# Kernel tuning notes

Hardware: AMD Instinct MI355X
Metric: run time of the kernel (lower is better)

The kernel has to match this reference:

```python
import jax, jax.numpy as jnp
import numpy as np

B, T, C, NH = 8, 512, 512, 8
HD = C // NH

def _layernorm(x, g, b, eps=1e-5):
    mu = jnp.mean(x, axis=-1, keepdims=True)
    var = jnp.var(x, axis=-1, keepdims=True)
    return (x - mu) * jax.lax.rsqrt(var + eps) * g + b

def setup_inputs() -> dict:
    key = jax.random.key(0)
    ks = jax.random.split(key, 5)
    return {
        "x": jax.random.normal(ks[0], (B, T, C), jnp.float32),
        "w_attn": jax.random.normal(ks[1], (3 * C, C), jnp.float32) * (1.0 / np.sqrt(C)),
        "b_attn": jnp.zeros((3 * C,), jnp.float32),
        "w_proj": jax.random.normal(ks[2], (C, C), jnp.float32) * (1.0 / np.sqrt(C)),
        "b_proj": jnp.zeros((C,), jnp.float32),
        "q_gamma": jnp.ones((C,), jnp.float32),
        "q_beta": jnp.zeros((C,), jnp.float32),
        "k_gamma": jnp.ones((C,), jnp.float32),
        "k_beta": jnp.zeros((C,), jnp.float32),
        "rel_emb": jax.random.normal(ks[3], (T, C), jnp.float32) * 0.02,
    }

def reference(x, w_attn, b_attn, w_proj, b_proj, q_gamma, q_beta, k_gamma, k_beta, rel_emb):
    b, t, c = x.shape
    # QKV projection (torch Linear: x @ W.T + b)
    qkv = x @ w_attn.T + b_attn                       # [B,T,3C]
    q, k, v = jnp.split(qkv, 3, axis=-1)
    # per-stream LayerNorm over full embedding dim (q_ln/k_ln = LayerNorm(n_embd))
    q = _layernorm(q, q_gamma, q_beta)
    k = _layernorm(k, k_gamma, k_beta)
    # split heads -> [B,NH,T,HD]
    q = q.reshape(b, t, NH, HD).transpose(0, 2, 1, 3)
    k = k.reshape(b, t, NH, HD).transpose(0, 2, 1, 3)
    v = v.reshape(b, t, NH, HD).transpose(0, 2, 1, 3)
    # relative-position bias: gather rel_emb[|i-j|] -> [T,T,NH,HD]
    idx = jnp.abs(jnp.arange(t)[None, :] - jnp.arange(t)[:, None])  # [T,T] int
    rel = rel_emb[idx].reshape(t, t, NH, HD)
    rel_bias = jnp.einsum("bhqd,qkhd->bhqk", q, rel)  # [B,NH,T,T]
    scale = 1.0 / np.sqrt(HD)
    scores = (jnp.einsum("bhqd,bhkd->bhqk", q, k) + rel_bias) * scale
    causal = jnp.tril(jnp.ones((t, t), bool))
    scores = jnp.where(causal[None, None], scores, jnp.finfo(scores.dtype).min)
    att = jax.nn.softmax(scores, axis=-1)
    y = jnp.einsum("bhqk,bhkd->bhqd", att, v)         # [B,NH,T,HD]
    y = y.transpose(0, 2, 1, 3).reshape(b, t, c)
    return y @ w_proj.T + b_proj
```

## Files before the change

kernel.cpp:

```cpp
#include <hip/hip_runtime.h>
#include <hip/hip_bf16.h>
#include <cstddef>

#define BB 8
#define TT 512
#define CC 512
#define NHH 8
#define HDD 64

typedef __attribute__((ext_vector_type(8))) short short8;
typedef __attribute__((ext_vector_type(4))) float f32x4;

__device__ __forceinline__ unsigned short f2bf(float f) {
    unsigned u = __float_as_uint(f);
    u += 0x7FFFu + ((u >> 16) & 1u);
    return (unsigned short)(u >> 16);
}
__device__ __forceinline__ float bf2f(unsigned short h) {
    return __uint_as_float(((unsigned)h) << 16);
}

__global__ __launch_bounds__(256) void cvt_all_k(
    const float* __restrict__ x, const float* __restrict__ wa,
    const float* __restrict__ wp, const float* __restrict__ rel,
    unsigned short* __restrict__ Xb, unsigned short* __restrict__ Wqb,
    unsigned short* __restrict__ Wpb, unsigned short* __restrict__ Relb)
{
    const int bidx = blockIdx.x;
    const float* in;
    unsigned short* out;
    int base;
    if (bidx < 2048)      { in = x;   out = Xb;   base = bidx; }
    else if (bidx < 2816) { in = wa;  out = Wqb;  base = bidx - 2048; }
    else if (bidx < 3072) { in = wp;  out = Wpb;  base = bidx - 2816; }
    else                  { in = rel; out = Relb; base = bidx - 3072; }
    const int i = base * 1024 + threadIdx.x * 4;
    const float4 v = *(const float4*)(in + i);
    unsigned short tmp[4] = {f2bf(v.x), f2bf(v.y), f2bf(v.z), f2bf(v.w)};
    *(uint2*)(out + i) = *(const uint2*)tmp;
}

__global__ __launch_bounds__(256, 2) void gemm_qkv_mfma(
    const unsigned short* __restrict__ Xb, const unsigned short* __restrict__ Wb,
    const float* __restrict__ bias, unsigned short* __restrict__ qkbuf,
    unsigned short* __restrict__ VT)
{
    __shared__ __align__(16) unsigned short lds[128 * 136];

    const int tid = threadIdx.x;
    const int w = tid >> 6, lane = tid & 63;
    const int c = lane & 15, quad = lane >> 4;
    const int wm = w >> 1, wn = w & 1;
    const int bm = blockIdx.y * 128, bn = blockIdx.x * 128;

    const unsigned short* pp[8];
#pragma unroll
    for (int l = 0; l < 8; ++l) {
        const int ci = w * 8 + l;
        if (ci < 16) {
            const int m16 = ci >> 1, kk = ci & 1;
            pp[l] = Xb + (size_t)(bm + m16 * 16 + c) * 512 + kk * 32 + quad * 8;
        } else {
            const int cb = ci - 16, n16 = cb >> 1, kk = cb & 1;
            pp[l] = Wb + (size_t)(bn + n16 * 16 + c) * 512 + kk * 32 + quad * 8;
        }
    }

    f32x4 acc[4][4];
#pragma unroll
    for (int i = 0; i < 4; ++i)
#pragma unroll
        for (int j = 0; j < 4; ++j) acc[i][j] = (f32x4){0.f, 0.f, 0.f, 0.f};

    short8 pre[8];
#pragma unroll
    for (int l = 0; l < 8; ++l) pre[l] = *(const short8*)pp[l];

    for (int k0 = 0; k0 < 512; k0 += 64) {
        __syncthreads();
#pragma unroll
        for (int l = 0; l < 8; ++l)
            *(short8*)&lds[(w * 8 + l) * 512 + lane * 8] = pre[l];
        __syncthreads();
        if (k0 + 64 < 512) {
#pragma unroll
            for (int l = 0; l < 8; ++l)
                pre[l] = *(const short8*)(pp[l] + k0 + 64);
        }
#pragma unroll
        for (int kk = 0; kk < 2; ++kk) {
            short8 af[4], bfr[4];
#pragma unroll
            for (int i = 0; i < 4; ++i)
                af[i] = *(const short8*)&lds[((wm * 4 + i) * 2 + kk) * 512 + lane * 8];
#pragma unroll
            for (int j = 0; j < 4; ++j)
                bfr[j] = *(const short8*)&lds[(16 + (wn * 4 + j) * 2 + kk) * 512 + lane * 8];
#pragma unroll
            for (int i = 0; i < 4; ++i)
#pragma unroll
                for (int j = 0; j < 4; ++j)
                    acc[i][j] = __builtin_amdgcn_mfma_f32_16x16x32_bf16(
                        af[i], bfr[j], acc[i][j], 0, 0, 0);
        }
    }

    float bj[4];
#pragma unroll
    for (int j = 0; j < 4; ++j) bj[j] = bias[bn + wn * 64 + j * 16 + c];

    if (bn < 1024) {
#pragma unroll
        for (int i = 0; i < 4; ++i)
#pragma unroll
            for (int j = 0; j < 4; ++j) {
                const int n = bn + wn * 64 + j * 16 + c;
#pragma unroll
                for (int r = 0; r < 4; ++r) {
                    const int m = bm + wm * 64 + i * 16 + quad * 4 + r;
                    qkbuf[(size_t)m * 1024 + n] = f2bf(acc[i][j][r] + bj[j]);
                }
            }
    } else {
        __syncthreads();
#pragma unroll
        for (int i = 0; i < 4; ++i)
#pragma unroll
            for (int j = 0; j < 4; ++j) {
                const int col = wn * 64 + j * 16 + c;
                const int row0 = wm * 64 + i * 16 + quad * 4;
                unsigned short t4[4];
#pragma unroll
                for (int r = 0; r < 4; ++r) t4[r] = f2bf(acc[i][j][r] + bj[j]);
                *(uint2*)&lds[col * 136 + row0] = *(const uint2*)t4;
            }
        __syncthreads();
        const int bi = bm >> 9, tb = bm & 511;
        const int hd0 = bn - 1024;
#pragma unroll
        for (int l = 0; l < 8; ++l) {
            const int idx = l * 256 + tid;
            const int col = idx >> 4, grp = idx & 15;
            const short8 v = *(const short8*)&lds[col * 136 + grp * 8];
            const int hd = hd0 + col, h = hd >> 6, d = hd & 63;
            *(short8*)(VT + ((size_t)(bi * NHH + h) * HDD + d) * TT + tb + grp * 8) = v;
        }
    }
}

__global__ __launch_bounds__(256) void ln_k(
    const unsigned short* __restrict__ qkbuf,
    const float* __restrict__ qg, const float* __restrict__ qb,
    const float* __restrict__ kg, const float* __restrict__ kb,
    unsigned short* __restrict__ Qh, unsigned short* __restrict__ Kh)
{
    const int wv = threadIdx.x >> 6, lane = threadIdx.x & 63;
    const int row = blockIdx.x * 4 + wv;
    const int bi = row >> 9, t = row & 511;
    const unsigned short* base = qkbuf + (size_t)row * 1024;

#pragma unroll
    for (int s = 0; s < 2; ++s) {
        const short8 v8 = *(const short8*)(base + s * 512 + lane * 8);
        float vf[8];
#pragma unroll
        for (int i = 0; i < 8; ++i) vf[i] = bf2f(((const unsigned short*)&v8)[i]);
        float sum = 0.f, sq = 0.f;
#pragma unroll
        for (int i = 0; i < 8; ++i) { sum += vf[i]; sq += vf[i] * vf[i]; }
#pragma unroll
        for (int off = 1; off < 64; off <<= 1) {
            sum += __shfl_xor(sum, off);
            sq += __shfl_xor(sq, off);
        }
        const float mu = sum * (1.f / 512.f);
        const float var = sq * (1.f / 512.f) - mu * mu;
        const float rsg = rsqrtf(var + 1e-5f);
        const float* gam = (s ? kg : qg) + lane * 8;
        const float* bet = (s ? kb : qb) + lane * 8;
        const float4 g0 = *(const float4*)gam, g1 = *(const float4*)(gam + 4);
        const float4 b0 = *(const float4*)bet, b1 = *(const float4*)(bet + 4);
        const float gv[8] = {g0.x, g0.y, g0.z, g0.w, g1.x, g1.y, g1.z, g1.w};
        const float bv[8] = {b0.x, b0.y, b0.z, b0.w, b1.x, b1.y, b1.z, b1.w};
        const float osc = s ? 1.0f : 0.125f;
        unsigned short o8[8];
#pragma unroll
        for (int i = 0; i < 8; ++i)
            o8[i] = f2bf(((vf[i] - mu) * rsg * gv[i] + bv[i]) * osc);
        unsigned short* outp = s ? Kh : Qh;
        *(short8*)(outp + ((size_t)(bi * NHH + (lane >> 3)) * TT + t) * HDD
                   + (lane & 7) * 8) = *(const short8*)o8;
    }
}

#define RD_BODY(nr_)                                                            \
    {                                                                           \
        const short8 br0 = *(const short8*)&Rels[((nr_) * 2 + 0) * 512 + lane * 8]; \
        const short8 br1 = *(const short8*)&Rels[((nr_) * 2 + 1) * 512 + lane * 8]; \
        f32x4 a2 = (f32x4){0.f, 0.f, 0.f, 0.f};                                 \
        a2 = __builtin_amdgcn_mfma_f32_16x16x32_bf16(aq0, br0, a2, 0, 0, 0);    \
        a2 = __builtin_amdgcn_mfma_f32_16x16x32_bf16(aq1, br1, a2, 0, 0, 0);    \
        const int colw = (mbase + (nr_) * 16 + c) & 127;                        \
        _Pragma("unroll")                                                       \
        for (int r = 0; r < 4; ++r)                                             \
            RDs[w][(quad * 4 + r) * 132 + colw] = f2bf(a2[r]);                  \
    }

__global__ __launch_bounds__(256, 2) void attn_k(
    const unsigned short* __restrict__ Qh, const unsigned short* __restrict__ Kh,
    const unsigned short* __restrict__ VT, const unsigned short* __restrict__ Relb,
    unsigned short* __restrict__ Yb)
{
    __shared__ __align__(16) unsigned short Ks[8 * 512];
    __shared__ __align__(16) unsigned short Vs[8 * 512];
    __shared__ __align__(16) unsigned short Rels[16 * 512];
    __shared__ __align__(16) unsigned short Ps[4][16 * 72];
    __shared__ __align__(16) unsigned short RDs[4][16 * 132];

    const int tid = threadIdx.x;
    const int w = tid >> 6;
    const int lane = tid & 63;
    const int c = lane & 15;
    const int quad = lane >> 4;

    const int bid = blockIdx.x;
    const int bit0 = bid & 1, bit8 = (bid >> 8) & 1;
    const int s_ = bit0 ^ bit8;
    const int q0 = (bid >> 1) & 7;
    const int qt = s_ ? 7 - q0 : q0;
    const int h = (bid >> 4) & 7;
    const int b = ((bid >> 7) & 1) | (bit8 << 1) | (bit0 << 2);
    const int i0 = qt * 64;

    const unsigned short* Qbase = Qh + (size_t)(b * NHH + h) * TT * HDD;
    const unsigned short* Kbase = Kh + (size_t)(b * NHH + h) * TT * HDD;
    const unsigned short* Vbase = VT + (size_t)(b * NHH + h) * HDD * TT;
    const unsigned short* Rbase = Relb + h * HDD;

    const unsigned short* qp = Qbase + (size_t)(i0 + w * 16 + c) * HDD + quad * 8;
    const short8 aq0 = *(const short8*)qp;
    const short8 aq1 = *(const short8*)(qp + 32);

#pragma unroll
    for (int kk = 0; kk < 2; ++kk) {
        const unsigned short* gp = Kbase + (size_t)(w * 16 + c) * HDD + kk * 32 + quad * 8;
        *(short8*)&Ks[(w * 2 + kk) * 512 + lane * 8] = *(const short8*)gp;
    }
#pragma unroll
    for (int js = 0; js < 2; ++js) {
        const unsigned short* gp = Vbase + (size_t)(w * 16 + c) * TT + js * 32 + quad * 8;
        *(short8*)&Vs[(w * 2 + js) * 512 + lane * 8] = *(const short8*)gp;
    }
    {
        const int mb0 = i0 - 63;
#pragma unroll
        for (int sb = 0; sb < 2; ++sb) {
#pragma unroll
            for (int kk = 0; kk < 2; ++kk) {
                const int n16 = w * 2 + sb;
                int mrow = mb0 + n16 * 16 + c;
                mrow = mrow < 0 ? 0 : (mrow > 511 ? 511 : mrow);
                *(short8*)&Rels[(n16 * 2 + kk) * 512 + lane * 8] =
                    *(const short8*)(Rbase + (size_t)mrow * CC + kk * 32 + quad * 8);
            }
        }
    }

    f32x4 oacc[4];
    float m_i[4], l_i[4];
#pragma unroll
    for (int r = 0; r < 4; ++r) { m_i[r] = -1e30f; l_i[r] = 0.f; }
#pragma unroll
    for (int nd = 0; nd < 4; ++nd) oacc[nd] = (f32x4){0.f, 0.f, 0.f, 0.f};

    __syncthreads();

    for (int jt = 0; jt <= qt; ++jt) {
        const int j0 = jt * 64;

        short8 pK0, pK1, pV0, pV1, pR0, pR1;
        if (jt < qt) {
            const int j1 = j0 + 64;
            const unsigned short* kp = Kbase + (size_t)(j1 + w * 16 + c) * HDD + quad * 8;
            pK0 = *(const short8*)kp;
            pK1 = *(const short8*)(kp + 32);
            const unsigned short* vp = Vbase + (size_t)(w * 16 + c) * TT + j1 + quad * 8;
            pV0 = *(const short8*)vp;
            pV1 = *(const short8*)(vp + 32);
            int mr = i0 - j1 - 63 + w * 16 + c;
            mr = mr < 0 ? 0 : (mr > 511 ? 511 : mr);
            const unsigned short* rp = Rbase + (size_t)mr * CC + quad * 8;
            pR0 = *(const short8*)rp;
            pR1 = *(const short8*)(rp + 32);
        }

        f32x4 sAcc[4];
#pragma unroll
        for (int ns = 0; ns < 4; ++ns) {
            const short8 bk0 = *(const short8*)&Ks[(ns * 2 + 0) * 512 + lane * 8];
            const short8 bk1 = *(const short8*)&Ks[(ns * 2 + 1) * 512 + lane * 8];
            f32x4 a2 = (f32x4){0.f, 0.f, 0.f, 0.f};
            a2 = __builtin_amdgcn_mfma_f32_16x16x32_bf16(aq0, bk0, a2, 0, 0, 0);
            a2 = __builtin_amdgcn_mfma_f32_16x16x32_bf16(aq1, bk1, a2, 0, 0, 0);
            sAcc[ns] = a2;
        }
        const int mbase = i0 - j0 - 63;
        if (jt == 0) {
#pragma unroll
            for (int nr = 0; nr < 8; ++nr) RD_BODY(nr)
        } else {
#pragma unroll
            for (int nr = 0; nr < 4; ++nr) RD_BODY(nr)
        }

        const int dbase = i0 - j0;
        float sc[4][4];
#pragma unroll
        for (int ns = 0; ns < 4; ++ns) {
#pragma unroll
            for (int r = 0; r < 4; ++r) {
                const int r16 = quad * 4 + r;
                const int jc = ns * 16 + c;
                const int dp = (dbase + w * 16 + r16 - jc) & 127;
                const float rdv = bf2f(RDs[w][r16 * 132 + dp]);
                sc[ns][r] = sAcc[ns][r] + rdv;
            }
        }
        if (jt == qt) {
#pragma unroll
            for (int ns = 0; ns < 4; ++ns)
#pragma unroll
                for (int r = 0; r < 4; ++r)
                    if (ns * 16 + c > w * 16 + quad * 4 + r) sc[ns][r] = -1e30f;
        }

        float alpha[4];
#pragma unroll
        for (int r = 0; r < 4; ++r) {
            float m = fmaxf(fmaxf(sc[0][r], sc[1][r]), fmaxf(sc[2][r], sc[3][r]));
#pragma unroll
            for (int off = 1; off < 16; off <<= 1) m = fmaxf(m, __shfl_xor(m, off));
            const float mn = fmaxf(m_i[r], m);
            alpha[r] = __expf(m_i[r] - mn);
            m_i[r] = mn;
        }
        float rs[4] = {0.f, 0.f, 0.f, 0.f};
#pragma unroll
        for (int ns = 0; ns < 4; ++ns) {
#pragma unroll
            for (int r = 0; r < 4; ++r) {
                const float p = __expf(sc[ns][r] - m_i[r]);
                rs[r] += p;
                Ps[w][(quad * 4 + r) * 72 + ns * 16 + c] = f2bf(p);
            }
        }
#pragma unroll
        for (int r = 0; r < 4; ++r) {
#pragma unroll
            for (int off = 1; off < 16; off <<= 1) rs[r] += __shfl_xor(rs[r], off);
            l_i[r] = l_i[r] * alpha[r] + rs[r];
        }
#pragma unroll
        for (int nd = 0; nd < 4; ++nd)
#pragma unroll
            for (int r = 0; r < 4; ++r) oacc[nd][r] *= alpha[r];

        const short8 ap0 = *(const short8*)&Ps[w][c * 72 + 0 * 32 + quad * 8];
        const short8 ap1 = *(const short8*)&Ps[w][c * 72 + 1 * 32 + quad * 8];
#pragma unroll
        for (int nd = 0; nd < 4; ++nd) {
            const short8 bv0 = *(const short8*)&Vs[(nd * 2 + 0) * 512 + lane * 8];
            const short8 bv1 = *(const short8*)&Vs[(nd * 2 + 1) * 512 + lane * 8];
            oacc[nd] = __builtin_amdgcn_mfma_f32_16x16x32_bf16(ap0, bv0, oacc[nd], 0, 0, 0);
            oacc[nd] = __builtin_amdgcn_mfma_f32_16x16x32_bf16(ap1, bv1, oacc[nd], 0, 0, 0);
        }

        if (jt < qt) {
            __syncthreads();
#pragma unroll
            for (int kk = 0; kk < 2; ++kk)
                *(short8*)&Ks[(w * 2 + kk) * 512 + lane * 8] = (kk ? pK1 : pK0);
#pragma unroll
            for (int js = 0; js < 2; ++js)
                *(short8*)&Vs[(w * 2 + js) * 512 + lane * 8] = (js ? pV1 : pV0);
#pragma unroll
            for (int kk = 0; kk < 2; ++kk)
                *(short8*)&Rels[(w * 2 + kk) * 512 + lane * 8] = (kk ? pR1 : pR0);
            __syncthreads();
        }
    }

#pragma unroll
    for (int r = 0; r < 4; ++r) {
        const float inv = 1.f / l_i[r];
        const int trow = i0 + w * 16 + quad * 4 + r;
        unsigned short* yb = Yb + ((size_t)b * TT + trow) * CC + h * HDD;
#pragma unroll
        for (int nd = 0; nd < 4; ++nd)
            yb[nd * 16 + c] = f2bf(oacc[nd][r] * inv);
    }
}

__global__ __launch_bounds__(256, 2) void gemm_proj_mfma(
    const unsigned short* __restrict__ Yb, const unsigned short* __restrict__ Wp,
    const float* __restrict__ bias, float* __restrict__ out)
{
    __shared__ __align__(16) unsigned short lds[24 * 512];

    const int tid = threadIdx.x;
    const int w = tid >> 6, lane = tid & 63;
    const int c = lane & 15, quad = lane >> 4;
    const int wm = w >> 1, wn = w & 1;
    const int bm = blockIdx.y * 64, bn = blockIdx.x * 128;

    const unsigned short* pp[6];
#pragma unroll
    for (int l = 0; l < 6; ++l) {
        const int ci = w * 6 + l;
        if (ci < 8) {
            const int m16 = ci >> 1, kk = ci & 1;
            pp[l] = Yb + (size_t)(bm + m16 * 16 + c) * 512 + kk * 32 + quad * 8;
        } else {
            const int cb = ci - 8, n16 = cb >> 1, kk = cb & 1;
            pp[l] = Wp + (size_t)(bn + n16 * 16 + c) * 512 + kk * 32 + quad * 8;
        }
    }

    f32x4 acc[2][4];
#pragma unroll
    for (int i = 0; i < 2; ++i)
#pragma unroll
        for (int j = 0; j < 4; ++j) acc[i][j] = (f32x4){0.f, 0.f, 0.f, 0.f};

    short8 pre[6];
#pragma unroll
    for (int l = 0; l < 6; ++l) pre[l] = *(const short8*)pp[l];

    for (int k0 = 0; k0 < 512; k0 += 64) {
        __syncthreads();
#pragma unroll
        for (int l = 0; l < 6; ++l)
            *(short8*)&lds[(w * 6 + l) * 512 + lane * 8] = pre[l];
        __syncthreads();
        if (k0 + 64 < 512) {
#pragma unroll
            for (int l = 0; l < 6; ++l)
                pre[l] = *(const short8*)(pp[l] + k0 + 64);
        }
#pragma unroll
        for (int kk = 0; kk < 2; ++kk) {
            short8 af[2], bfr[4];
#pragma unroll
            for (int i = 0; i < 2; ++i)
                af[i] = *(const short8*)&lds[((wm * 2 + i) * 2 + kk) * 512 + lane * 8];
#pragma unroll
            for (int j = 0; j < 4; ++j)
                bfr[j] = *(const short8*)&lds[(8 + (wn * 4 + j) * 2 + kk) * 512 + lane * 8];
#pragma unroll
            for (int i = 0; i < 2; ++i)
#pragma unroll
                for (int j = 0; j < 4; ++j)
                    acc[i][j] = __builtin_amdgcn_mfma_f32_16x16x32_bf16(
                        af[i], bfr[j], acc[i][j], 0, 0, 0);
        }
    }

#pragma unroll
    for (int j = 0; j < 4; ++j) {
        const int n = bn + wn * 64 + j * 16 + c;
        const float bj = bias[n];
#pragma unroll
        for (int i = 0; i < 2; ++i)
#pragma unroll
            for (int r = 0; r < 4; ++r) {
                const int m = bm + wm * 32 + i * 16 + quad * 4 + r;
                out[(size_t)m * 512 + n] = acc[i][j][r] + bj;
            }
    }
}

extern "C" void kernel_launch(void* const* d_in, const int* in_sizes, int n_in,
                              void* d_out, int out_size, void* d_ws, size_t ws_size,
                              hipStream_t stream)
{
    const float* x      = (const float*)d_in[0];
    const float* w_attn = (const float*)d_in[1];
    const float* b_attn = (const float*)d_in[2];
    const float* w_proj = (const float*)d_in[3];
    const float* b_proj = (const float*)d_in[4];
    const float* q_g    = (const float*)d_in[5];
    const float* q_b    = (const float*)d_in[6];
    const float* k_g    = (const float*)d_in[7];
    const float* k_b    = (const float*)d_in[8];
    const float* rel    = (const float*)d_in[9];
    float* out = (float*)d_out;

    unsigned short* qkbuf = (unsigned short*)d_ws;
    unsigned short* Qh   = qkbuf + (size_t)4096 * 1024;
    unsigned short* Kh   = Qh + (size_t)4096 * 512;
    unsigned short* VT   = Kh + (size_t)4096 * 512;
    unsigned short* Relb = VT + (size_t)4096 * 512;
    unsigned short* Xb   = Relb + (size_t)512 * 512;
    unsigned short* Wqb  = Xb + (size_t)4096 * 512;
    unsigned short* Wpb  = Wqb + (size_t)1536 * 512;
    unsigned short* Yb   = qkbuf;

    cvt_all_k<<<3328, 256, 0, stream>>>(x, w_attn, w_proj, rel, Xb, Wqb, Wpb, Relb);
    gemm_qkv_mfma<<<dim3(12, 32), 256, 0, stream>>>(Xb, Wqb, b_attn, qkbuf, VT);
    ln_k<<<1024, 256, 0, stream>>>(qkbuf, q_g, q_b, k_g, k_b, Qh, Kh);
    attn_k<<<512, 256, 0, stream>>>(Qh, Kh, VT, Relb, Yb);
    gemm_proj_mfma<<<dim3(4, 64), 256, 0, stream>>>(Yb, Wpb, b_proj, out);
}
```

Before: 139.5 us.

## Fuse QKV GEMM with LayerNorm and fp32 X conversion, restructure projection GEMM

Drops the separate X bf16 conversion and the LayerNorm kernel. The new QKV kernel reads fp32 x, converts it in-register while staging into LDS, and loads B fragments straight from global memory into registers with double buffering. Each block computes a full 512-wide stream slab so it can apply LayerNorm (including the softmax scale folded with log2e) before writing Q/K/VT. The attention softmax switches to exp2f to match that folded scale, and the projection GEMM is restructured the same way. The cost is fewer, heavier blocks (192 blocks at 1 per CU) with high register pressure, which risks lower occupancy.

New measurement: 144.3 us. +3.4%, slower.

```diff
diff --git a/kernel.cpp b/kernel.cpp
--- a/kernel.cpp
+++ b/kernel.cpp
@@ -20,176 +20,238 @@
     return __uint_as_float(((unsigned)h) << 16);
 }
 
-__global__ __launch_bounds__(256) void cvt_all_k(
-    const float* __restrict__ x, const float* __restrict__ wa,
-    const float* __restrict__ wp, const float* __restrict__ rel,
-    unsigned short* __restrict__ Xb, unsigned short* __restrict__ Wqb,
-    unsigned short* __restrict__ Wpb, unsigned short* __restrict__ Relb)
+__global__ __launch_bounds__(256) void cvt_w_k(
+    const float* __restrict__ wa, const float* __restrict__ wp,
+    const float* __restrict__ rel,
+    unsigned short* __restrict__ Wqb, unsigned short* __restrict__ Wpb,
+    unsigned short* __restrict__ Relb)
 {
     const int bidx = blockIdx.x;
     const float* in;
     unsigned short* out;
     int base;
-    if (bidx < 2048)      { in = x;   out = Xb;   base = bidx; }
-    else if (bidx < 2816) { in = wa;  out = Wqb;  base = bidx - 2048; }
-    else if (bidx < 3072) { in = wp;  out = Wpb;  base = bidx - 2816; }
-    else                  { in = rel; out = Relb; base = bidx - 3072; }
+    if (bidx < 768)       { in = wa;  out = Wqb;  base = bidx; }
+    else if (bidx < 1024) { in = wp;  out = Wpb;  base = bidx - 768; }
+    else                  { in = rel; out = Relb; base = bidx - 1024; }
     const int i = base * 1024 + threadIdx.x * 4;
     const float4 v = *(const float4*)(in + i);
     unsigned short tmp[4] = {f2bf(v.x), f2bf(v.y), f2bf(v.z), f2bf(v.w)};
     *(uint2*)(out + i) = *(const uint2*)tmp;
 }
 
-__global__ __launch_bounds__(256, 2) void gemm_qkv_mfma(
-    const unsigned short* __restrict__ Xb, const unsigned short* __restrict__ Wb,
-    const float* __restrict__ bias, unsigned short* __restrict__ qkbuf,
+#define QSTAGE_A()                                                            \
+    __syncthreads();                                                          \
+    _Pragma("unroll")                                                         \
+    for (int l = 0; l < 2; ++l) {                                             \
+        unsigned short t8[8];                                                 \
+        _Pragma("unroll")                                                     \
+        for (int e = 0; e < 4; ++e) {                                         \
+            t8[e] = f2bf(ap[l][0][e]);                                        \
+            t8[4 + e] = f2bf(ap[l][1][e]);                                    \
+        }                                                                     \
+        *(short8*)&smem[dstA[l]] = *(const short8*)t8;                        \
+    }                                                                         \
+    __syncthreads();
+
+#define QLOADA(koff)                                                          \
+    _Pragma("unroll")                                                         \
+    for (int l = 0; l < 2; ++l) {                                             \
+        ap[l][0] = *(const f32x4*)(srcA[l] + (koff));                         \
+        ap[l][1] = *(const f32x4*)(srcA[l] + (koff) + 4);                     \
+    }
+
+#define QLOADB(bN, koff)                                                      \
+    _Pragma("unroll")                                                         \
+    for (int kk = 0; kk < 2; ++kk)                                            \
+        _Pragma("unroll")                                                     \
+        for (int j = 0; j < 8; ++j)                                           \
+            bN[kk * 8 + j] =                                                  \
+                *(const short8*)(Bb + (size_t)j * 8192 + kk * 32 + (koff));
+
+#define QCOMPUTE(bN)                                                          \
+    _Pragma("unroll")                                                         \
+    for (int kk = 0; kk < 2; ++kk) {                                          \
+        short8 af[4];                                                         \
+        _Pragma("unroll")                                                     \
+        for (int i = 0; i < 4; ++i)                                           \
+            af[i] = *(const short8*)&smem[((i << 1) | kk) * 512 + lane * 8];  \
+        _Pragma("unroll")                                                     \
+        for (int j = 0; j < 8; ++j)                                           \
+            _Pragma("unroll")                                                 \
+            for (int i = 0; i < 4; ++i)                                       \
+                acc[i][j] = __builtin_amdgcn_mfma_f32_16x16x32_bf16(          \
+                    af[i], bN[kk * 8 + j], acc[i][j], 0, 0, 0);               \
+    }
+
+__global__ __launch_bounds__(256, 1) void qkvln_k(
+    const float* __restrict__ x, const unsigned short* __restrict__ Wqb,
+    const float* __restrict__ b_attn,
+    const float* __restrict__ qg, const float* __restrict__ qb,
+    const float* __restrict__ kg, const float* __restrict__ kb,
+    unsigned short* __restrict__ Qh, unsigned short* __restrict__ Kh,
     unsigned short* __restrict__ VT)
 {
-    __shared__ __align__(16) unsigned short lds[128 * 136];
+    __shared__ __align__(16) unsigned short smem[512 * 68];
 
     const int tid = threadIdx.x;
     const int w = tid >> 6, lane = tid & 63;
     const int c = lane & 15, quad = lane >> 4;
-    const int wm = w >> 1, wn = w & 1;
-    const int bm = blockIdx.y * 128, bn = blockIdx.x * 128;
-
-    const unsigned short* pp[8];
-#pragma unroll
-    for (int l = 0; l < 8; ++l) {
-        const int ci = w * 8 + l;
-        if (ci < 16) {
-            const int m16 = ci >> 1, kk = ci & 1;
-            pp[l] = Xb + (size_t)(bm + m16 * 16 + c) * 512 + kk * 32 + quad * 8;
-        } else {
-            const int cb = ci - 16, n16 = cb >> 1, kk = cb & 1;
-            pp[l] = Wb + (size_t)(bn + n16 * 16 + c) * 512 + kk * 32 + quad * 8;
-        }
-    }
-
-    f32x4 acc[4][4];
+
+    const int strm = blockIdx.x >> 6;
+    const int slab = blockIdx.x & 63;
+    const int row0 = slab * 64;
+    const int bi = row0 >> 9, trow0 = row0 & 511;
+
+    const float* srcA[2];
+    int dstA[2];
+#pragma unroll
+    for (int l = 0; l < 2; ++l) {
+        const int idx = l * 256 + tid;
+        const int fr = idx >> 6, li = idx & 63;
+        srcA[l] = x + (size_t)(row0 + (fr >> 1) * 16 + (li & 15)) * 512
+                    + (fr & 1) * 32 + (li >> 4) * 8;
+        dstA[l] = fr * 512 + li * 8;
+    }
+    const unsigned short* Bb =
+        Wqb + (size_t)(strm * 512 + w * 128 + c) * 512 + quad * 8;
+
+    f32x4 acc[4][8];
 #pragma unroll
     for (int i = 0; i < 4; ++i)
 #pragma unroll
-        for (int j = 0; j < 4; ++j) acc[i][j] = (f32x4){0.f, 0.f, 0.f, 0.f};
-
-    short8 pre[8];
-#pragma unroll
-    for (int l = 0; l < 8; ++l) pre[l] = *(const short8*)pp[l];
-
-    for (int k0 = 0; k0 < 512; k0 += 64) {
+        for (int j = 0; j < 8; ++j) acc[i][j] = (f32x4){0.f, 0.f, 0.f, 0.f};
+
+    f32x4 ap[2][2];
+    short8 b0[16], b1[16];
+    QLOADA(0);
+    QLOADB(b0, 0);
+
+#pragma unroll
+    for (int kp = 0; kp < 4; ++kp) {
+        const int ka = kp * 128;
+        QSTAGE_A();
+        QLOADA(ka + 64);
+        QLOADB(b1, ka + 64);
+        QCOMPUTE(b0);
+        QSTAGE_A();
+        if (kp < 3) {
+            QLOADA(ka + 128);
+            QLOADB(b0, ka + 128);
+        }
+        QCOMPUTE(b1);
+    }
+
+    {
+        const int gcb = strm * 512 + w * 128;
+#pragma unroll
+        for (int j = 0; j < 8; ++j) {
+            const float bj = b_attn[gcb + j * 16 + c];
+#pragma unroll
+            for (int i = 0; i < 4; ++i)
+#pragma unroll
+                for (int r = 0; r < 4; ++r) acc[i][j][r] += bj;
+        }
+    }
+
+    if (strm < 2) {
+        float s1[4][4], s2[4][4];
+#pragma unroll
+        for (int i = 0; i < 4; ++i)
+#pragma unroll
+            for (int r = 0; r < 4; ++r) {
+                float a1 = 0.f, a2 = 0.f;
+#pragma unroll
+                for (int j = 0; j < 8; ++j) {
+                    const float v = acc[i][j][r];
+                    a1 += v;
+                    a2 += v * v;
+                }
+#pragma unroll
+                for (int off = 1; off < 16; off <<= 1) {
+                    a1 += __shfl_xor(a1, off);
+                    a2 += __shfl_xor(a2, off);
+                }
+                s1[i][r] = a1;
+                s2[i][r] = a2;
+            }
         __syncthreads();
-#pragma unroll
-        for (int l = 0; l < 8; ++l)
-            *(short8*)&lds[(w * 8 + l) * 512 + lane * 8] = pre[l];
+        if (c == 0) {
+#pragma unroll
+            for (int i = 0; i < 4; ++i)
+#pragma unroll
+                for (int r = 0; r < 4; ++r)
+                    ((float2*)smem)[w * 64 + i * 16 + quad * 4 + r] =
+                        make_float2(s1[i][r], s2[i][r]);
+        }
         __syncthreads();
-        if (k0 + 64 < 512) {
-#pragma unroll
-            for (int l = 0; l < 8; ++l)
-                pre[l] = *(const short8*)(pp[l] + k0 + 64);
-        }
-#pragma unroll
-        for (int kk = 0; kk < 2; ++kk) {
-            short8 af[4], bfr[4];
+        float rsg[4][4], nmu[4][4];
+#pragma unroll
+        for (int i = 0; i < 4; ++i)
+#pragma unroll
+            for (int r = 0; r < 4; ++r) {
+                float a1 = 0.f, a2 = 0.f;
+#pragma unroll
+                for (int ww = 0; ww < 4; ++ww) {
+                    const float2 t =
+                        ((const float2*)smem)[ww * 64 + i * 16 + quad * 4 + r];
+                    a1 += t.x;
+                    a2 += t.y;
+                }
+                const float mu = a1 * (1.f / 512.f);
+                const float var = a2 * (1.f / 512.f) - mu * mu;
+                const float rs = rsqrtf(var + 1e-5f);
+                rsg[i][r] = rs;
+                nmu[i][r] = -mu * rs;
+            }
+        const float osc = (strm == 0) ? 0.1803368801f : 1.0f;
+        const float* gam = (strm == 0) ? qg : kg;
+        const float* bet = (strm == 0) ? qb : kb;
+        float gv[8], bv[8];
+#pragma unroll
+        for (int j = 0; j < 8; ++j) {
+            gv[j] = gam[w * 128 + j * 16 + c] * osc;
+            bv[j] = bet[w * 128 + j * 16 + c] * osc;
+        }
+        unsigned short* op =
+            ((strm == 0) ? Qh : Kh) + (size_t)bi * (NHH * TT * HDD);
+#pragma unroll
+        for (int j = 0; j < 8; ++j) {
+            const int gc = w * 128 + j * 16 + c;
+            unsigned short* opc =
+                op + (size_t)(gc >> 6) * (TT * HDD) + (gc & 63);
 #pragma unroll
             for (int i = 0; i < 4; ++i)
-                af[i] = *(const short8*)&lds[((wm * 4 + i) * 2 + kk) * 512 + lane * 8];
-#pragma unroll
-            for (int j = 0; j < 4; ++j)
-                bfr[j] = *(const short8*)&lds[(16 + (wn * 4 + j) * 2 + kk) * 512 + lane * 8];
-#pragma unroll
-            for (int i = 0; i < 4; ++i)
-#pragma unroll
-                for (int j = 0; j < 4; ++j)
-                    acc[i][j] = __builtin_amdgcn_mfma_f32_16x16x32_bf16(
-                        af[i], bfr[j], acc[i][j], 0, 0, 0);
-        }
-    }
-
-    float bj[4];
-#pragma unroll
-    for (int j = 0; j < 4; ++j) bj[j] = bias[bn + wn * 64 + j * 16 + c];
-
-    if (bn < 1024) {
-#pragma unroll
-        for (int i = 0; i < 4; ++i)
-#pragma unroll
-            for (int j = 0; j < 4; ++j) {
-                const int n = bn + wn * 64 + j * 16 + c;
 #pragma unroll
                 for (int r = 0; r < 4; ++r) {
-                    const int m = bm + wm * 64 + i * 16 + quad * 4 + r;
-                    qkbuf[(size_t)m * 1024 + n] = f2bf(acc[i][j][r] + bj[j]);
+                    const int trow = trow0 + i * 16 + quad * 4 + r;
+                    const float t = fmaf(acc[i][j][r], rsg[i][r], nmu[i][r]);
+                    opc[(size_t)trow * HDD] = f2bf(fmaf(t, gv[j], bv[j]));
                 }
-            }
+        }
     } else {
         __syncthreads();
 #pragma unroll
         for (int i = 0; i < 4; ++i)
 #pragma unroll
-            for (int j = 0; j < 4; ++j) {
-                const int col = wn * 64 + j * 16 + c;
-                const int row0 = wm * 64 + i * 16 + quad * 4;
+            for (int j = 0; j < 8; ++j) {
+                const int col = w * 128 + j * 16 + c;
+                const int rowt = i * 16 + quad * 4;
                 unsigned short t4[4];
 #pragma unroll
-                for (int r = 0; r < 4; ++r) t4[r] = f2bf(acc[i][j][r] + bj[j]);
-                *(uint2*)&lds[col * 136 + row0] = *(const uint2*)t4;
+                for (int r = 0; r < 4; ++r) t4[r] = f2bf(acc[i][j][r]);
+                *(uint2*)&smem[col * 68 + rowt] = *(const uint2*)t4;
             }
         __syncthreads();
-        const int bi = bm >> 9, tb = bm & 511;
-        const int hd0 = bn - 1024;
-#pragma unroll
-        for (int l = 0; l < 8; ++l) {
+#pragma unroll
+        for (int l = 0; l < 16; ++l) {
             const int idx = l * 256 + tid;
-            const int col = idx >> 4, grp = idx & 15;
-            const short8 v = *(const short8*)&lds[col * 136 + grp * 8];
-            const int hd = hd0 + col, h = hd >> 6, d = hd & 63;
-            *(short8*)(VT + ((size_t)(bi * NHH + h) * HDD + d) * TT + tb + grp * 8) = v;
-        }
-    }
-}
-
-__global__ __launch_bounds__(256) void ln_k(
-    const unsigned short* __restrict__ qkbuf,
-    const float* __restrict__ qg, const float* __restrict__ qb,
-    const float* __restrict__ kg, const float* __restrict__ kb,
-    unsigned short* __restrict__ Qh, unsigned short* __restrict__ Kh)
-{
-    const int wv = threadIdx.x >> 6, lane = threadIdx.x & 63;
-    const int row = blockIdx.x * 4 + wv;
-    const int bi = row >> 9, t = row & 511;
-    const unsigned short* base = qkbuf + (size_t)row * 1024;
-
-#pragma unroll
-    for (int s = 0; s < 2; ++s) {
-        const short8 v8 = *(const short8*)(base + s * 512 + lane * 8);
-        float vf[8];
-#pragma unroll
-        for (int i = 0; i < 8; ++i) vf[i] = bf2f(((const unsigned short*)&v8)[i]);
-        float sum = 0.f, sq = 0.f;
-#pragma unroll
-        for (int i = 0; i < 8; ++i) { sum += vf[i]; sq += vf[i] * vf[i]; }
-#pragma unroll
-        for (int off = 1; off < 64; off <<= 1) {
-            sum += __shfl_xor(sum, off);
-            sq += __shfl_xor(sq, off);
-        }
-        const float mu = sum * (1.f / 512.f);
-        const float var = sq * (1.f / 512.f) - mu * mu;
-        const float rsg = rsqrtf(var + 1e-5f);
-        const float* gam = (s ? kg : qg) + lane * 8;
-        const float* bet = (s ? kb : qb) + lane * 8;
-        const float4 g0 = *(const float4*)gam, g1 = *(const float4*)(gam + 4);
-        const float4 b0 = *(const float4*)bet, b1 = *(const float4*)(bet + 4);
-        const float gv[8] = {g0.x, g0.y, g0.z, g0.w, g1.x, g1.y, g1.z, g1.w};
-        const float bv[8] = {b0.x, b0.y, b0.z, b0.w, b1.x, b1.y, b1.z, b1.w};
-        const float osc = s ? 1.0f : 0.125f;
-        unsigned short o8[8];
-#pragma unroll
-        for (int i = 0; i < 8; ++i)
-            o8[i] = f2bf(((vf[i] - mu) * rsg * gv[i] + bv[i]) * osc);
-        unsigned short* outp = s ? Kh : Qh;
-        *(short8*)(outp + ((size_t)(bi * NHH + (lane >> 3)) * TT + t) * HDD
-                   + (lane & 7) * 8) = *(const short8*)o8;
+            const int col = idx >> 3, part = idx & 7;
+            const uint2 lo = *(const uint2*)&smem[col * 68 + part * 8];
+            const uint2 hi = *(const uint2*)&smem[col * 68 + part * 8 + 4];
+            uint2 pair[2] = {lo, hi};
+            *(short8*)(VT + ((size_t)(bi * NHH + (col >> 6)) * HDD + (col & 63)) * TT
+                       + trow0 + part * 8) = *(const short8*)pair;
+        }
     }
 }
 
@@ -341,7 +403,7 @@
 #pragma unroll
             for (int off = 1; off < 16; off <<= 1) m = fmaxf(m, __shfl_xor(m, off));
             const float mn = fmaxf(m_i[r], m);
-            alpha[r] = __expf(m_i[r] - mn);
+            alpha[r] = exp2f(m_i[r] - mn);
             m_i[r] = mn;
         }
         float rs[4] = {0.f, 0.f, 0.f, 0.f};
@@ -349,7 +411,7 @@
         for (int ns = 0; ns < 4; ++ns) {
 #pragma unroll
             for (int r = 0; r < 4; ++r) {
-                const float p = __expf(sc[ns][r] - m_i[r]);
+                const float p = exp2f(sc[ns][r] - m_i[r]);
                 rs[r] += p;
                 Ps[w][(quad * 4 + r) * 72 + ns * 16 + c] = f2bf(p);
             }
@@ -401,30 +463,53 @@
     }
 }
 
-__global__ __launch_bounds__(256, 2) void gemm_proj_mfma(
-    const unsigned short* __restrict__ Yb, const unsigned short* __restrict__ Wp,
+#define PLOADB(bN, koff)                                                      \
+    _Pragma("unroll")                                                         \
+    for (int kk = 0; kk < 2; ++kk)                                            \
+        _Pragma("unroll")                                                     \
+        for (int j = 0; j < 4; ++j)                                           \
+            bN[kk * 4 + j] =                                                  \
+                *(const short8*)(Bb + (size_t)j * 8192 + kk * 32 + (koff));
+
+#define PSTAGE_A()                                                            \
+    __syncthreads();                                                          \
+    *(short8*)&Alds[dstA] = apre;                                             \
+    __syncthreads();
+
+#define PCOMPUTE(bN)                                                          \
+    _Pragma("unroll")                                                         \
+    for (int kk = 0; kk < 2; ++kk) {                                          \
+        short8 af[2];                                                         \
+        _Pragma("unroll")                                                     \
+        for (int i = 0; i < 2; ++i)                                           \
+            af[i] = *(const short8*)&Alds[((i << 1) | kk) * 512 + lane * 8];  \
+        _Pragma("unroll")                                                     \
+        for (int j = 0; j < 4; ++j)                                           \
+            _Pragma("unroll")                                                 \
+            for (int i = 0; i < 2; ++i)                                       \
+                acc[i][j] = __builtin_amdgcn_mfma_f32_16x16x32_bf16(          \
+                    af[i], bN[kk * 4 + j], acc[i][j], 0, 0, 0);               \
+    }
+
+__global__ __launch_bounds__(256, 1) void gemm_proj_k(
+    const unsigned short* __restrict__ Yb, const unsigned short* __restrict__ Wpb,
     const float* __restrict__ bias, float* __restrict__ out)
 {
-    __shared__ __align__(16) unsigned short lds[24 * 512];
+    __shared__ __align__(16) unsigned short Alds[4 * 512];
 
     const int tid = threadIdx.x;
     const int w = tid >> 6, lane = tid & 63;
     const int c = lane & 15, quad = lane >> 4;
-    const int wm = w >> 1, wn = w & 1;
-    const int bm = blockIdx.y * 64, bn = blockIdx.x * 128;
-
-    const unsigned short* pp[6];
-#pragma unroll
-    for (int l = 0; l < 6; ++l) {
-        const int ci = w * 6 + l;
-        if (ci < 8) {
-            const int m16 = ci >> 1, kk = ci & 1;
-            pp[l] = Yb + (size_t)(bm + m16 * 16 + c) * 512 + kk * 32 + quad * 8;
-        } else {
-            const int cb = ci - 8, n16 = cb >> 1, kk = cb & 1;
-            pp[l] = Wp + (size_t)(bn + n16 * 16 + c) * 512 + kk * 32 + quad * 8;
-        }
-    }
+    const int colh = blockIdx.x >> 7, slab = blockIdx.x & 127;
+    const int row0 = slab * 32;
+    const int ncol0 = colh * 256 + w * 64;
+
+    const int fr = tid >> 6, li = tid & 63;
+    const unsigned short* srcA =
+        Yb + (size_t)(row0 + (fr >> 1) * 16 + (li & 15)) * 512
+           + (fr & 1) * 32 + (li >> 4) * 8;
+    const int dstA = fr * 512 + li * 8;
+    const unsigned short* Bb = Wpb + (size_t)(ncol0 + c) * 512 + quad * 8;
 
     f32x4 acc[2][4];
 #pragma unroll
@@ -432,50 +517,35 @@
 #pragma unroll
         for (int j = 0; j < 4; ++j) acc[i][j] = (f32x4){0.f, 0.f, 0.f, 0.f};
 
-    short8 pre[6];
-#pragma unroll
-    for (int l = 0; l < 6; ++l) pre[l] = *(const short8*)pp[l];
-
-    for (int k0 = 0; k0 < 512; k0 += 64) {
-        __syncthreads();
-#pragma unroll
-        for (int l = 0; l < 6; ++l)
-            *(short8*)&lds[(w * 6 + l) * 512 + lane * 8] = pre[l];
-        __syncthreads();
-        if (k0 + 64 < 512) {
-#pragma unroll
-            for (int l = 0; l < 6; ++l)
-                pre[l] = *(const short8*)(pp[l] + k0 + 64);
-        }
-#pragma unroll
-        for (int kk = 0; kk < 2; ++kk) {
-            short8 af[2], bfr[4];
-#pragma unroll
-            for (int i = 0; i < 2; ++i)
-                af[i] = *(const short8*)&lds[((wm * 2 + i) * 2 + kk) * 512 + lane * 8];
-#pragma unroll
-            for (int j = 0; j < 4; ++j)
-                bfr[j] = *(const short8*)&lds[(8 + (wn * 4 + j) * 2 + kk) * 512 + lane * 8];
-#pragma unroll
-            for (int i = 0; i < 2; ++i)
-#pragma unroll
-                for (int j = 0; j < 4; ++j)
-                    acc[i][j] = __builtin_amdgcn_mfma_f32_16x16x32_bf16(
-                        af[i], bfr[j], acc[i][j], 0, 0, 0);
-        }
+    short8 apre = *(const short8*)srcA;
+    short8 b0[8], b1[8];
+    PLOADB(b0, 0);
+
+#pragma unroll
+    for (int kp = 0; kp < 4; ++kp) {
+        const int ka = kp * 128;
+        PSTAGE_A();
+        if (true) { apre = *(const short8*)(srcA + ka + 64); }
+        PLOADB(b1, ka + 64);
+        PCOMPUTE(b0);
+        PSTAGE_A();
+        if (kp < 3) {
+            apre = *(const short8*)(srcA + ka + 128);
+            PLOADB(b0, ka + 128);
+        }
+        PCOMPUTE(b1);
     }
 
 #pragma unroll
     for (int j = 0; j < 4; ++j) {
-        const int n = bn + wn * 64 + j * 16 + c;
-        const float bj = bias[n];
+        const int gc = ncol0 + j * 16 + c;
+        const float bj = bias[gc];
 #pragma unroll
         for (int i = 0; i < 2; ++i)
 #pragma unroll
-            for (int r = 0; r < 4; ++r) {
-                const int m = bm + wm * 32 + i * 16 + quad * 4 + r;
-                out[(size_t)m * 512 + n] = acc[i][j][r] + bj;
-            }
+            for (int r = 0; r < 4; ++r)
+                out[(size_t)(row0 + i * 16 + quad * 4 + r) * 512 + gc] =
+                    acc[i][j][r] + bj;
     }
 }
 
@@ -495,19 +565,16 @@
     const float* rel    = (const float*)d_in[9];
     float* out = (float*)d_out;
 
-    unsigned short* qkbuf = (unsigned short*)d_ws;
-    unsigned short* Qh   = qkbuf + (size_t)4096 * 1024;
+    unsigned short* Qh   = (unsigned short*)d_ws;
     unsigned short* Kh   = Qh + (size_t)4096 * 512;
     unsigned short* VT   = Kh + (size_t)4096 * 512;
-    unsigned short* Relb = VT + (size_t)4096 * 512;
-    unsigned short* Xb   = Relb + (size_t)512 * 512;
-    unsigned short* Wqb  = Xb + (size_t)4096 * 512;
+    unsigned short* Yb   = VT + (size_t)4096 * 512;
+    unsigned short* Relb = Yb + (size_t)4096 * 512;
+    unsigned short* Wqb  = Relb + (size_t)512 * 512;
     unsigned short* Wpb  = Wqb + (size_t)1536 * 512;
-    unsigned short* Yb   = qkbuf;
-
-    cvt_all_k<<<3328, 256, 0, stream>>>(x, w_attn, w_proj, rel, Xb, Wqb, Wpb, Relb);
-    gemm_qkv_mfma<<<dim3(12, 32), 256, 0, stream>>>(Xb, Wqb, b_attn, qkbuf, VT);
-    ln_k<<<1024, 256, 0, stream>>>(qkbuf, q_g, q_b, k_g, k_b, Qh, Kh);
+
+    cvt_w_k<<<1280, 256, 0, stream>>>(w_attn, w_proj, rel, Wqb, Wpb, Relb);
+    qkvln_k<<<192, 256, 0, stream>>>(x, Wqb, b_attn, q_g, q_b, k_g, k_b, Qh, Kh, VT);
     attn_k<<<512, 256, 0, stream>>>(Qh, Kh, VT, Relb, Yb);
-    gemm_proj_mfma<<<dim3(4, 64), 256, 0, stream>>>(Yb, Wpb, b_proj, out);
-}
+    gemm_proj_k<<<256, 256, 0, stream>>>(Yb, Wpb, b_proj, out);
+}
```
